# Performance work log

Measured on AMD Instinct MI355X. Metric: run time of the kernel, lower is better.

Reference implementation:

```python
import jax, jax.numpy as jnp
import numpy as np

N_BRANCHES = 4
BATCH = 8192
DIM = 4096
NUM_CLASSES = 1024
MARGIN = 0.3
EPS = 1e-8


def setup_inputs() -> dict:
    key = jax.random.key(0)
    branch_feats = jax.random.normal(key, (N_BRANCHES, BATCH, DIM), dtype=jnp.float32)
    # every class appears BATCH // NUM_CLASSES = 8 times (>1, so no detach branch)
    targets = jnp.arange(BATCH, dtype=jnp.int32) % NUM_CLASSES
    return {"branch_feats": branch_feats, "targets": targets, "num_classes": NUM_CLASSES}


def _centers(branch_feats, targets, num_classes):
    # masked per-class mean == segment mean (torch.unique over 0..C-1, sorted)
    counts = jax.ops.segment_sum(jnp.ones(branch_feats.shape[1], jnp.float32),
                                 targets, num_segments=num_classes)  # [C]
    sums = jax.vmap(lambda f: jax.ops.segment_sum(f, targets, num_segments=num_classes))(
        branch_feats)  # [N, C, D]
    return sums / counts[None, :, None]


def reference(branch_feats, targets, num_classes):
    centers = _centers(branch_feats, targets, num_classes)  # [N, C, D]
    C = num_classes

    # hard negative per (branch, class): min_{l != k} ||c[k] - c[l]||
    sq = jnp.sum(centers * centers, axis=-1)                 # [N, C]
    gram = jnp.einsum('nkd,nld->nkl', centers, centers)      # [N, C, C]
    d2 = jnp.maximum(sq[:, :, None] + sq[:, None, :] - 2.0 * gram, 0.0)
    dist = jnp.sqrt(d2)                                      # [N, C, C]
    dist = jnp.where(jnp.eye(C, dtype=bool)[None], jnp.inf, dist)
    hard_neg = jnp.min(dist, axis=-1)                        # [N, C]

    # positive distances for each unordered branch pair i < j
    ii, jj = jnp.triu_indices(N_BRANCHES, k=1)
    # F.pairwise_distance adds eps to the difference before the norm
    pos = jnp.linalg.norm(centers[ii] - centers[jj] + EPS, axis=-1)  # [P, C]

    # loss += relu(margin + pos_dist[k] - hard_neg_i[k]); valid_pairs = P * C
    return jnp.mean(jax.nn.relu(MARGIN + pos - hard_neg[ii]))
```

## Files before the change

kernel.cpp:

```cpp
#include <hip/hip_runtime.h>

#define N_BR   4
#define BATCH  8192
#define DIM    4096
#define NCLS   1024
#define MARGIN 0.3f
#define EPS_P  1e-8f
#define MAXPC  16

typedef __attribute__((ext_vector_type(4))) float f32x4;
typedef __attribute__((ext_vector_type(2))) float f32x2;
typedef __attribute__((ext_vector_type(4))) int i32x4;
typedef unsigned char u8;

__global__ __launch_bounds__(256) void prepk(
    const int* __restrict__ targets, int* __restrict__ members,
    int* __restrict__ cnt, unsigned int* __restrict__ hn) {
  __shared__ int cnt_s[4], off_s[5];
  int c = blockIdx.x, tid = threadIdx.x;
  int w = tid >> 6, lane = tid & 63;
  if (tid < N_BR) hn[tid * NCLS + c] = 0x7F800000u;
  int cn = 0;
  for (int i = 0; i < (BATCH / 4) / 64; ++i) {
    int b = w * (BATCH / 4) + i * 64 + lane;
    cn += __popcll(__ballot(targets[b] == c));
  }
  if (lane == 0) cnt_s[w] = cn;
  __syncthreads();
  if (tid == 0) {
    off_s[0] = 0;
    for (int i = 0; i < 4; ++i) off_s[i + 1] = off_s[i] + cnt_s[i];
    cnt[c] = off_s[4];
  }
  __syncthreads();
  int pos = off_s[w];
  for (int i = 0; i < (BATCH / 4) / 64; ++i) {
    int b = w * (BATCH / 4) + i * 64 + lane;
    bool hit = (targets[b] == c);
    unsigned long long m = __ballot(hit);
    if (hit) {
      int p = pos + __popcll(m & ((1ULL << lane) - 1ULL));
      if (p < MAXPC) members[c * MAXPC + p] = b;
    }
    pos += __popcll(m);
  }
}

__global__ __launch_bounds__(256) void centersk(
    const float* __restrict__ feats, const int* __restrict__ members,
    const int* __restrict__ cnt, u8* __restrict__ cq,
    float* __restrict__ sq) {
  int c = blockIdx.x, n = blockIdx.y, tid = threadIdx.x;
  int count = cnt[c]; if (count > MAXPC) count = MAXPC;
  int beg = c * MAXPC, end = beg + count;
  float inv = 1.0f / (float)count;
  const float* fb = feats + (size_t)n * BATCH * DIM;
  size_t cbase = ((size_t)n * NCLS + c) * DIM;
  float ssq = 0.f;
#pragma unroll
  for (int it = 0; it < DIM / 1024; ++it) {
    int d = (it * 256 + tid) * 4;
    f32x4 acc = {0.f, 0.f, 0.f, 0.f};
    for (int m = beg; m < end; ++m) {
      int b = members[m];
      f32x4 v = *(const f32x4*)(fb + (size_t)b * DIM + d);
      acc += v;
    }
    f32x4 ctr = acc * inv;
    int packed = 0;
    packed = __builtin_amdgcn_cvt_pk_fp8_f32(ctr.x, ctr.y, packed, false);
    packed = __builtin_amdgcn_cvt_pk_fp8_f32(ctr.z, ctr.w, packed, true);
    *(int*)(cq + cbase + d) = packed;
    ssq += ctr.x * ctr.x + ctr.y * ctr.y + ctr.z * ctr.z + ctr.w * ctr.w;
  }
  for (int off = 1; off < 64; off <<= 1) ssq += __shfl_xor(ssq, off, 64);
  __shared__ float rs[4];
  if ((tid & 63) == 0) rs[tid >> 6] = ssq;
  __syncthreads();
  if (tid == 0) sq[n * NCLS + c] = rs[0] + rs[1] + rs[2] + rs[3];
}

__global__ __launch_bounds__(256) void gramk(
    const u8* __restrict__ cq, const float* __restrict__ sq,
    unsigned int* __restrict__ hn) {
  __shared__ u8 As[6][64 * 64];
  __shared__ u8 Bs[6][64 * 64];
  int x = (blockIdx.x & 7) * 17 + (blockIdx.x >> 3);
  int n = blockIdx.y;
  int ti = 0;
  while (x >= 16 - ti) { x -= 16 - ti; ++ti; }
  int tj = ti + x;
  int tid = threadIdx.x;
  int wid = tid >> 6, lane = tid & 63;
  int wr = wid >> 1, wc = wid & 1;
  int r0 = ti * 64, c0 = tj * 64;
  const u8* base = cq + (size_t)n * NCLS * DIM;

  f32x4 acc[2][2] = {};

#define STAGE(buf, kb)                                                          \
  {                                                                             \
    int g = tid;                              \
    int row_ = g >> 2, c16_ = g & 3;                                            \
    int sc16_ = c16_ ^ ((row_ >> 1) & 3);    \
    const u8* gA_ = base + (size_t)(r0 + row_) * DIM + (kb) + sc16_ * 16;       \
    const u8* gB_ = base + (size_t)(c0 + row_) * DIM + (kb) + sc16_ * 16;       \
    __builtin_amdgcn_global_load_lds(                                           \
        (const __attribute__((address_space(1))) void*)gA_,                     \
        (__attribute__((address_space(3))) void*)(As[buf] + g * 16), 16, 0, 0); \
    __builtin_amdgcn_global_load_lds(                                           \
        (const __attribute__((address_space(1))) void*)gB_,                     \
        (__attribute__((address_space(3))) void*)(Bs[buf] + g * 16), 16, 0, 0); \
  }

#define COMPUTE(buf)                                                            \
  {                                                                             \
    _Pragma("unroll")                                                           \
    for (int ks = 0; ks < 2; ++ks) {                                            \
      long a_[2], b_[2];                                                        \
      int co_ = ks * 4 + (lane >> 4);         \
      _Pragma("unroll")                                                         \
      for (int mi = 0; mi < 2; ++mi) {                                          \
        int r_ = wr * 32 + mi * 16 + (lane & 15);                               \
        int p_ = ((r_ >> 1) & 3) << 1;                                          \
        a_[mi] = *(const long*)(As[buf] + r_ * 64 + (co_ ^ p_) * 8);            \
      }                                                                         \
      _Pragma("unroll")                                                         \
      for (int nj = 0; nj < 2; ++nj) {                                          \
        int r_ = wc * 32 + nj * 16 + (lane & 15);                               \
        int p_ = ((r_ >> 1) & 3) << 1;                                          \
        b_[nj] = *(const long*)(Bs[buf] + r_ * 64 + (co_ ^ p_) * 8);            \
      }                                                                         \
      _Pragma("unroll")                                                         \
      for (int mi = 0; mi < 2; ++mi)                                            \
        _Pragma("unroll")                                                       \
        for (int nj = 0; nj < 2; ++nj)                                          \
          acc[mi][nj] = __builtin_amdgcn_mfma_f32_16x16x32_fp8_fp8(             \
              a_[mi], b_[nj], acc[mi][nj], 0, 0, 0);                            \
    }                                                                           \
  }

  const int NK = DIM / 64;
  STAGE(0, 0); STAGE(1, 64); STAGE(2, 128); STAGE(3, 192); STAGE(4, 256);
  int cb = 0, sb = 5;
  for (int k = 0; k < NK; ++k) {
    if (k < NK - 4)       asm volatile("s_waitcnt vmcnt(8)" ::: "memory");
    else if (k == NK - 4) asm volatile("s_waitcnt vmcnt(6)" ::: "memory");
    else if (k == NK - 3) asm volatile("s_waitcnt vmcnt(4)" ::: "memory");
    else if (k == NK - 2) asm volatile("s_waitcnt vmcnt(2)" ::: "memory");
    else                  asm volatile("s_waitcnt vmcnt(0)" ::: "memory");
    __builtin_amdgcn_s_barrier();
    if (k + 5 < NK) STAGE(sb, (k + 5) * 64);
    COMPUTE(cb);
    cb = (cb == 5) ? 0 : cb + 1;
    sb = (sb == 5) ? 0 : sb + 1;
  }
#undef STAGE
#undef COMPUTE

  const float* sqn = sq + n * NCLS;
  unsigned int* hb = hn + n * NCLS;
  int grp = lane >> 4, lid = lane & 15;
  float d2v[2][2][4];
#pragma unroll
  for (int mi = 0; mi < 2; ++mi)
#pragma unroll
    for (int nj = 0; nj < 2; ++nj)
#pragma unroll
      for (int j = 0; j < 4; ++j) {
        int rr = r0 + wr * 32 + mi * 16 + grp * 4 + j;
        int cc = c0 + wc * 32 + nj * 16 + lid;
        float d2 = fmaxf(sqn[rr] + sqn[cc] - 2.0f * acc[mi][nj][j], 0.f);
        d2v[mi][nj][j] = (rr == cc) ? __builtin_inff() : d2;
      }
#pragma unroll
  for (int mi = 0; mi < 2; ++mi)
#pragma unroll
    for (int j = 0; j < 4; ++j) {
      float dmin = fminf(d2v[mi][0][j], d2v[mi][1][j]);
#pragma unroll
      for (int off = 1; off < 16; off <<= 1)
        dmin = fminf(dmin, __shfl_xor(dmin, off, 64));
      if (lid == 0) {
        int rr = r0 + wr * 32 + mi * 16 + grp * 4 + j;
        atomicMin(&hb[rr], __float_as_uint(dmin));
      }
    }
#pragma unroll
  for (int nj = 0; nj < 2; ++nj) {
    float cmin = __builtin_inff();
#pragma unroll
    for (int mi = 0; mi < 2; ++mi)
#pragma unroll
      for (int j = 0; j < 4; ++j)
        cmin = fminf(cmin, d2v[mi][nj][j]);
    cmin = fminf(cmin, __shfl_xor(cmin, 16, 64));
    cmin = fminf(cmin, __shfl_xor(cmin, 32, 64));
    if (grp == 0) {
      int cc = c0 + wc * 32 + nj * 16 + lid;
      atomicMin(&hb[cc], __float_as_uint(cmin));
    }
  }
}

__global__ __launch_bounds__(256) void posk(
    const u8* __restrict__ cq, const unsigned int* __restrict__ hn,
    float* __restrict__ partial) {
  int c = blockIdx.x, tid = threadIdx.x;
  const int ii[6] = {0, 0, 0, 1, 1, 2};
  const int jj[6] = {1, 2, 3, 2, 3, 3};
  float v[N_BR][16];
#pragma unroll
  for (int nb = 0; nb < N_BR; ++nb) {
    i32x4 wds = *(const i32x4*)(cq + ((size_t)nb * NCLS + c) * DIM + tid * 16);
#pragma unroll
    for (int q = 0; q < 4; ++q) {
      f32x2 lo = __builtin_amdgcn_cvt_pk_f32_fp8(wds[q], false);
      f32x2 hi = __builtin_amdgcn_cvt_pk_f32_fp8(wds[q], true);
      v[nb][q * 4 + 0] = lo.x; v[nb][q * 4 + 1] = lo.y;
      v[nb][q * 4 + 2] = hi.x; v[nb][q * 4 + 3] = hi.y;
    }
  }
  float s[6];
#pragma unroll
  for (int p = 0; p < 6; ++p) {
    float t = 0.f;
#pragma unroll
    for (int e = 0; e < 16; ++e) {
      float df = v[ii[p]][e] - v[jj[p]][e] + EPS_P;
      t += df * df;
    }
    s[p] = t;
  }
  __shared__ float red[4][6];
#pragma unroll
  for (int p = 0; p < 6; ++p) {
    float x = s[p];
    for (int off = 1; off < 64; off <<= 1) x += __shfl_xor(x, off, 64);
    if ((tid & 63) == 0) red[tid >> 6][p] = x;
  }
  __syncthreads();
  if (tid == 0) {
    float total = 0.f;
#pragma unroll
    for (int p = 0; p < 6; ++p) {
      float sum = red[0][p] + red[1][p] + red[2][p] + red[3][p];
      float pos = sqrtf(sum);
      float hneg = sqrtf(__uint_as_float(hn[ii[p] * NCLS + c]));
      float t = MARGIN + pos - hneg;
      total += fmaxf(t, 0.f);
    }
    partial[c] = total;
  }
}

__global__ void finalk(const float* __restrict__ partial, float* __restrict__ out) {
  int tid = threadIdx.x;
  float s = 0.f;
  for (int c = tid; c < NCLS; c += 256) s += partial[c];
  for (int off = 1; off < 64; off <<= 1) s += __shfl_xor(s, off, 64);
  __shared__ float rs[4];
  if ((tid & 63) == 0) rs[tid >> 6] = s;
  __syncthreads();
  if (tid == 0) out[0] = (rs[0] + rs[1] + rs[2] + rs[3]) * (1.0f / (6.0f * NCLS));
}

extern "C" void kernel_launch(void* const* d_in, const int* in_sizes, int n_in,
                              void* d_out, int out_size, void* d_ws, size_t ws_size,
                              hipStream_t stream) {
  const float* feats = (const float*)d_in[0];
  const int* targets = (const int*)d_in[1];
  float* out = (float*)d_out;
  char* ws = (char*)d_ws;

  int* members     = (int*)(ws + 0);
  int* cnt         = (int*)(ws + 65536);
  float* sq        = (float*)(ws + 69632);
  unsigned int* hn = (unsigned int*)(ws + 86016);
  float* partial   = (float*)(ws + 102400);
  u8* cq           = (u8*)(ws + 131072);

  hipLaunchKernelGGL(prepk, dim3(NCLS), dim3(256), 0, stream,
                     targets, members, cnt, hn);
  hipLaunchKernelGGL(centersk, dim3(NCLS, N_BR), dim3(256), 0, stream,
                     feats, members, cnt, cq, sq);
  hipLaunchKernelGGL(gramk, dim3(136, N_BR), dim3(256), 0, stream, cq, sq, hn);
  hipLaunchKernelGGL(posk, dim3(NCLS), dim3(256), 0, stream, cq, hn, partial);
  hipLaunchKernelGGL(finalk, dim3(1), dim3(256), 0, stream, partial, out);
}
```

Measured before the change: 161.0 us.

## Restructure center accumulation loop and widen gram K-tile with shallower pipeline

The centers kernel now loops over class members on the outside and keeps four float4 accumulators, so each member row is read with four independent loads instead of re-reading the members array per chunk. The gram kernel switches from 64-byte K slices with a 6-deep buffer ring to 128-byte slices with a 3-deep ring, halving the number of barriers and waitcnt steps while each stage issues two loads per thread. This trades prefetch depth for fewer synchronisation points and more MFMA work per iteration. The swizzle still XORs only over four 16-byte chunks inside a 128-byte row, which may leave some LDS bank conflicts.

Result: slower. 167.3 us (+3.9%).

```diff
diff --git a/kernel.cpp b/kernel.cpp
--- a/kernel.cpp
+++ b/kernel.cpp
@@ -52,21 +52,25 @@
     float* __restrict__ sq) {
   int c = blockIdx.x, n = blockIdx.y, tid = threadIdx.x;
   int count = cnt[c]; if (count > MAXPC) count = MAXPC;
-  int beg = c * MAXPC, end = beg + count;
+  int beg = c * MAXPC;
   float inv = 1.0f / (float)count;
   const float* fb = feats + (size_t)n * BATCH * DIM;
   size_t cbase = ((size_t)n * NCLS + c) * DIM;
+  f32x4 acc[4] = {};
+  for (int m = 0; m < count; ++m) {
+    int b = members[beg + m];
+    const float* rp = fb + (size_t)b * DIM;
+#pragma unroll
+    for (int it = 0; it < 4; ++it) {
+      int d = (it * 256 + tid) * 4;
+      acc[it] += *(const f32x4*)(rp + d);
+    }
+  }
   float ssq = 0.f;
 #pragma unroll
-  for (int it = 0; it < DIM / 1024; ++it) {
+  for (int it = 0; it < 4; ++it) {
     int d = (it * 256 + tid) * 4;
-    f32x4 acc = {0.f, 0.f, 0.f, 0.f};
-    for (int m = beg; m < end; ++m) {
-      int b = members[m];
-      f32x4 v = *(const f32x4*)(fb + (size_t)b * DIM + d);
-      acc += v;
-    }
-    f32x4 ctr = acc * inv;
+    f32x4 ctr = acc[it] * inv;
     int packed = 0;
     packed = __builtin_amdgcn_cvt_pk_fp8_f32(ctr.x, ctr.y, packed, false);
     packed = __builtin_amdgcn_cvt_pk_fp8_f32(ctr.z, ctr.w, packed, true);
@@ -83,8 +87,8 @@
 __global__ __launch_bounds__(256) void gramk(
     const u8* __restrict__ cq, const float* __restrict__ sq,
     unsigned int* __restrict__ hn) {
-  __shared__ u8 As[6][64 * 64];
-  __shared__ u8 Bs[6][64 * 64];
+  __shared__ u8 As[3][64 * 128];
+  __shared__ u8 Bs[3][64 * 128];
   int x = (blockIdx.x & 7) * 17 + (blockIdx.x >> 3);
   int n = blockIdx.y;
   int ti = 0;
@@ -100,36 +104,39 @@
 
 #define STAGE(buf, kb)                                                          \
   {                                                                             \
-    int g = tid;                              \
-    int row_ = g >> 2, c16_ = g & 3;                                            \
-    int sc16_ = c16_ ^ ((row_ >> 1) & 3);    \
-    const u8* gA_ = base + (size_t)(r0 + row_) * DIM + (kb) + sc16_ * 16;       \
-    const u8* gB_ = base + (size_t)(c0 + row_) * DIM + (kb) + sc16_ * 16;       \
-    __builtin_amdgcn_global_load_lds(                                           \
-        (const __attribute__((address_space(1))) void*)gA_,                     \
-        (__attribute__((address_space(3))) void*)(As[buf] + g * 16), 16, 0, 0); \
-    __builtin_amdgcn_global_load_lds(                                           \
-        (const __attribute__((address_space(1))) void*)gB_,                     \
-        (__attribute__((address_space(3))) void*)(Bs[buf] + g * 16), 16, 0, 0); \
+    _Pragma("unroll")                                                           \
+    for (int it_ = 0; it_ < 2; ++it_) {                                         \
+      int g = it_ * 256 + tid;                \
+      int row_ = g >> 3, c16_ = g & 7;                                          \
+      int sc16_ = c16_ ^ ((row_ >> 1) & 3);      \
+      const u8* gA_ = base + (size_t)(r0 + row_) * DIM + (kb) + sc16_ * 16;     \
+      const u8* gB_ = base + (size_t)(c0 + row_) * DIM + (kb) + sc16_ * 16;     \
+      __builtin_amdgcn_global_load_lds(                                         \
+          (const __attribute__((address_space(1))) void*)gA_,                   \
+          (__attribute__((address_space(3))) void*)(As[buf] + g * 16), 16, 0, 0);\
+      __builtin_amdgcn_global_load_lds(                                         \
+          (const __attribute__((address_space(1))) void*)gB_,                   \
+          (__attribute__((address_space(3))) void*)(Bs[buf] + g * 16), 16, 0, 0);\
+    }                                                                           \
   }
 
 #define COMPUTE(buf)                                                            \
   {                                                                             \
     _Pragma("unroll")                                                           \
-    for (int ks = 0; ks < 2; ++ks) {                                            \
+    for (int ks = 0; ks < 4; ++ks) {                                            \
       long a_[2], b_[2];                                                        \
-      int co_ = ks * 4 + (lane >> 4);         \
+      int co_ = ks * 4 + (lane >> 4);       \
       _Pragma("unroll")                                                         \
       for (int mi = 0; mi < 2; ++mi) {                                          \
         int r_ = wr * 32 + mi * 16 + (lane & 15);                               \
         int p_ = ((r_ >> 1) & 3) << 1;                                          \
-        a_[mi] = *(const long*)(As[buf] + r_ * 64 + (co_ ^ p_) * 8);            \
+        a_[mi] = *(const long*)(As[buf] + r_ * 128 + (co_ ^ p_) * 8);           \
       }                                                                         \
       _Pragma("unroll")                                                         \
       for (int nj = 0; nj < 2; ++nj) {                                          \
         int r_ = wc * 32 + nj * 16 + (lane & 15);                               \
         int p_ = ((r_ >> 1) & 3) << 1;                                          \
-        b_[nj] = *(const long*)(Bs[buf] + r_ * 64 + (co_ ^ p_) * 8);            \
+        b_[nj] = *(const long*)(Bs[buf] + r_ * 128 + (co_ ^ p_) * 8);           \
       }                                                                         \
       _Pragma("unroll")                                                         \
       for (int mi = 0; mi < 2; ++mi)                                            \
@@ -140,20 +147,14 @@
     }                                                                           \
   }
 
-  const int NK = DIM / 64;
-  STAGE(0, 0); STAGE(1, 64); STAGE(2, 128); STAGE(3, 192); STAGE(4, 256);
-  int cb = 0, sb = 5;
+  const int NK = DIM / 128;
+  STAGE(0, 0); STAGE(1, 128);
   for (int k = 0; k < NK; ++k) {
-    if (k < NK - 4)       asm volatile("s_waitcnt vmcnt(8)" ::: "memory");
-    else if (k == NK - 4) asm volatile("s_waitcnt vmcnt(6)" ::: "memory");
-    else if (k == NK - 3) asm volatile("s_waitcnt vmcnt(4)" ::: "memory");
-    else if (k == NK - 2) asm volatile("s_waitcnt vmcnt(2)" ::: "memory");
-    else                  asm volatile("s_waitcnt vmcnt(0)" ::: "memory");
+    if (k < NK - 1) asm volatile("s_waitcnt vmcnt(4)" ::: "memory");
+    else            asm volatile("s_waitcnt vmcnt(0)" ::: "memory");
     __builtin_amdgcn_s_barrier();
-    if (k + 5 < NK) STAGE(sb, (k + 5) * 64);
-    COMPUTE(cb);
-    cb = (cb == 5) ? 0 : cb + 1;
-    sb = (sb == 5) ? 0 : sb + 1;
+    if (k + 2 < NK) STAGE((k + 2) % 3, (k + 2) * 128);
+    COMPUTE(k % 3);
   }
 #undef STAGE
 #undef COMPUTE
```
